# Performance work log

Hardware: AMD Instinct MI355X
Metric: run time of the kernel (lower is better)

The kernel has to match this reference:

```python
import jax, jax.numpy as jnp
import numpy as np

# --- static config (from init_kwargs) ---
B = 256        # num graphs
NPG = 128      # nodes per graph
EPG = 512      # edges per graph
DIN = 128      # dim_node
D = 256        # dim_hidden
RATIO = 0.5    # causal_ratio
N_RES = int(RATIO * EPG)
BN_EPS = 1e-5


def setup_inputs() -> dict:
    key = jax.random.key(0)
    ks = jax.random.split(key, 24)
    N = B * NPG
    x = jax.random.normal(ks[0], (N, DIN), jnp.float32)
    # edges confined within each graph, contiguous per graph (graph-sorted)
    src = jax.random.randint(ks[1], (B, EPG), 0, NPG)
    dst = jax.random.randint(ks[2], (B, EPG), 0, NPG)
    off = (jnp.arange(B, dtype=jnp.int32) * NPG)[:, None]
    edge_index = jnp.stack([(src + off).reshape(-1), (dst + off).reshape(-1)], 0).astype(jnp.int32)
    batch = jnp.repeat(jnp.arange(B, dtype=jnp.int32), NPG)

    s = 0.05
    def rn(k, shape):
        return jax.random.normal(k, shape, jnp.float32) * s
    p = dict(
        x=x, edge_index=edge_index, batch=batch,
        vemb=rn(ks[3], (1, D)),
        # conv1 GIN mlp: Linear(DIN,2D) -> BN -> ReLU -> Linear(2D,D)
        W1a=rn(ks[4], (DIN, 2 * D)), b1a=jnp.zeros((2 * D,)),
        g1a=jnp.ones((2 * D,)), be1a=jnp.zeros((2 * D,)),
        W1b=rn(ks[5], (2 * D, D)), b1b=jnp.zeros((D,)),
        g1=jnp.ones((D,)), be1=jnp.zeros((D,)),          # outer batch_norm1
        # conv2 GIN mlp
        W2a=rn(ks[6], (D, 2 * D)), b2a=jnp.zeros((2 * D,)),
        g2a=jnp.ones((2 * D,)), be2a=jnp.zeros((2 * D,)),
        W2b=rn(ks[7], (2 * D, D)), b2b=jnp.zeros((D,)),
        g2=jnp.ones((D,)), be2=jnp.zeros((D,)),          # outer batch_norm2
        # edge scorer: Linear(2D, 1)
        Wl=rn(ks[8], (2 * D, 1)), bl=jnp.zeros((1,)),
    )
    return p


def _bn(h, g, b):
    mu = h.mean(0)
    var = jnp.mean((h - mu) ** 2, 0)
    return (h - mu) * jax.lax.rsqrt(var + BN_EPS) * g + b


def reference(x, edge_index, batch, vemb,
              W1a, b1a, g1a, be1a, W1b, b1b, g1, be1,
              W2a, b2a, g2a, be2a, W2b, b2b, g2, be2,
              Wl, bl):
    N = x.shape[0]
    row, col = edge_index[0], edge_index[1]

    def gin(h, Wa, ba, ga, bta, Wb, bb):
        # GINConv, eps=0: mlp(h + sum_{j->i} h_j), aggregate src feats at dst
        agg = jax.ops.segment_sum(h[row], col, num_segments=N)
        z = (h + agg) @ Wa + ba
        z = jax.nn.relu(_bn(z, ga, bta))
        return z @ Wb + bb

    # layer 1: conv1 -> bn -> relu (dropout_rate = 0)
    post = jax.nn.relu(_bn(gin(x, W1a, b1a, g1a, be1a, W1b, b1b), g1, be1))
    # virtual node gather (embedding of index 0, one per graph)
    vfeat = jnp.broadcast_to(vemb[0], (B, D))
    post = post + vfeat[batch]
    # layer 2 (last): conv2 -> bn, no relu
    xn = _bn(gin(post, W2a, b2a, g2a, be2a, W2b, b2b), g2, be2)

    # edge scoring
    erep = jnp.concatenate([xn[row], xn[col]], axis=-1)          # [E, 2D]
    pred = (erep @ Wl + bl.astype(erep.dtype)).reshape(-1)       # [E]

    # per-graph top-k split (equal EPG edges per graph)
    pw = pred.reshape(B, EPG)
    order = jnp.argsort(-pw, axis=1)
    idx_r, idx_d = order[:, :N_RES], order[:, N_RES:]
    causal_w = jnp.take_along_axis(pw, idx_r, 1).reshape(-1)
    conf_w = -jnp.take_along_axis(pw, idx_d, 1).reshape(-1)
    ei = edge_index.reshape(2, B, EPG)
    causal_ei = jnp.take_along_axis(ei, jnp.broadcast_to(idx_r[None], (2, B, N_RES)), axis=2).reshape(2, -1)
    conf_ei = jnp.take_along_axis(ei, jnp.broadcast_to(idx_d[None], (2, B, EPG - N_RES)), axis=2).reshape(2, -1)
    return (causal_ei, causal_w, conf_ei, conf_w, pred)
```

## Files before the change

### kernel.cpp

```cpp
#include <hip/hip_runtime.h>

#define BGR   256
#define NPG   128
#define EPG   512
#define DIN   128
#define DD    256
#define DD2   512
#define NTOT  (BGR * NPG)
#define ETOT  (BGR * EPG)
#define NRES  (EPG / 2)
#define NCHUNK 256
#define MP    136

#define OFF_CEI  0
#define OFF_CW   (2 * BGR * NRES)
#define OFF_FEI  (OFF_CW + BGR * NRES)
#define OFF_FW   (OFF_FEI + 2 * BGR * NRES)
#define OFF_PRED (OFF_FW + BGR * NRES)

typedef unsigned short ushortt;
typedef __attribute__((ext_vector_type(4))) unsigned short us4;
typedef __attribute__((ext_vector_type(8))) unsigned short us8;
typedef __attribute__((ext_vector_type(8))) short short8;
typedef __attribute__((ext_vector_type(4))) float f32x4;

__device__ __forceinline__ ushortt f2bf(float f) {
    unsigned int u = __float_as_uint(f);
    unsigned int r = (u + 0x7fffu + ((u >> 16) & 1u)) >> 16;
    return (ushortt)r;
}
__device__ __forceinline__ float bf2f(ushortt u) {
    return __uint_as_float(((unsigned int)u) << 16);
}

__device__ __forceinline__ void g2lds16(const void* g, void* l) {
    __builtin_amdgcn_global_load_lds(
        (const __attribute__((address_space(1))) unsigned int*)g,
        (__attribute__((address_space(3))) unsigned int*)l, 16, 0, 0);
}

__global__ __launch_bounds__(256) void prep(const float* __restrict__ W1a,
                                            const float* __restrict__ W1b,
                                            const float* __restrict__ W2a,
                                            const float* __restrict__ W2b,
                                            const int* __restrict__ ei,
                                            ushortt* __restrict__ Wt1a,
                                            ushortt* __restrict__ Wt1b,
                                            ushortt* __restrict__ Wt2a,
                                            ushortt* __restrict__ Wt2b,
                                            ushortt* __restrict__ Madj) {
    __shared__ int cnt[NPG * NPG];
    const int t = threadIdx.x;
    if (blockIdx.x < 1792) {
        const int idx = blockIdx.x * 256 + t;
        if (idx < 65536) {
            const int k = idx >> 9, n = idx & 511;
            Wt1a[n * DIN + k] = f2bf(W1a[idx]);
        } else if (idx < 196608) {
            const int i = idx - 65536;
            const int k = i >> 8, n = i & 255;
            Wt1b[n * DD2 + k] = f2bf(W1b[i]);
        } else if (idx < 327680) {
            const int i = idx - 196608;
            const int k = i >> 9, n = i & 511;
            Wt2a[n * DD + k] = f2bf(W2a[i]);
        } else if (idx < 458752) {
            const int i = idx - 327680;
            const int k = i >> 8, n = i & 255;
            Wt2b[n * DD2 + k] = f2bf(W2b[i]);
        }
        return;
    }
    const int b = blockIdx.x - 1792;
    for (int i = t; i < NPG * NPG; i += 256) cnt[i] = 0;
    __syncthreads();
    for (int e = t; e < EPG; e += 256) {
        const int src = ei[b * EPG + e] - b * NPG;
        const int dst = ei[ETOT + b * EPG + e] - b * NPG;
        atomicAdd(&cnt[dst * NPG + src], 1);
    }
    __syncthreads();
#pragma unroll
    for (int k = 0; k < 8; ++k) {
        const int i0 = (t + k * 256) * 8;
        us8 o;
#pragma unroll
        for (int e = 0; e < 8; ++e) {
            const int i = i0 + e;
            const int v = cnt[i] + (((i >> 7) == (i & 127)) ? 1 : 0);
            o[e] = f2bf((float)v);
        }
        *(us8*)&Madj[(size_t)b * NPG * NPG + i0] = o;
    }
}

__global__ __launch_bounds__(256) void agg1_mm(const float* __restrict__ x,
                                               const ushortt* __restrict__ Madj,
                                               ushortt* __restrict__ s1) {
    __shared__ ushortt Ms[NPG * MP];
    __shared__ ushortt XT[DIN * MP];
    const int b = blockIdx.x, t = threadIdx.x;
    const int wave = t >> 6, lane = t & 63;
    const int qd = lane >> 4, r = lane & 15;
    const ushortt* Mg = Madj + (size_t)b * NPG * NPG;
#pragma unroll
    for (int k = 0; k < 8; ++k) {
        const int ch = t + k * 256;
        const int m = ch >> 4, sc = (ch & 15) * 8;
        *(us8*)&Ms[m * MP + sc] = *(const us8*)&Mg[m * NPG + sc];
    }
#pragma unroll 4
    for (int it = 0; it < 64; ++it) {
        const int s = it * 2 + (t >> 7);
        const int c = t & 127;
        XT[c * MP + s] = f2bf(x[(size_t)(b * NPG + s) * DIN + c]);
    }
    __syncthreads();
    const int wm = (wave >> 1) * 64, wn = (wave & 1) * 64;
    f32x4 acc[4][4] = {};
#pragma unroll
    for (int ks = 0; ks < 4; ++ks) {
        const int k0 = ks * 32 + qd * 8;
        short8 af[4], bfr[4];
#pragma unroll
        for (int i = 0; i < 4; ++i)
            af[i] = *(const short8*)&Ms[(wm + i * 16 + r) * MP + k0];
#pragma unroll
        for (int j = 0; j < 4; ++j)
            bfr[j] = *(const short8*)&XT[(wn + j * 16 + r) * MP + k0];
#pragma unroll
        for (int i = 0; i < 4; ++i)
#pragma unroll
            for (int j = 0; j < 4; ++j)
                acc[i][j] = __builtin_amdgcn_mfma_f32_16x16x32_bf16(af[i], bfr[j], acc[i][j], 0, 0, 0);
    }
    __syncthreads();
    ushortt* Cs = Ms;
#pragma unroll
    for (int j = 0; j < 4; ++j) {
        const int coll = wn + j * 16 + r;
#pragma unroll
        for (int i = 0; i < 4; ++i)
#pragma unroll
            for (int tt = 0; tt < 4; ++tt)
                Cs[(wm + i * 16 + qd * 4 + tt) * DIN + coll] = f2bf(acc[i][j][tt]);
    }
    __syncthreads();
#pragma unroll
    for (int k = 0; k < 8; ++k) {
        const int ch = t + k * 256;
        const int row = ch >> 4, colc = (ch & 15) * 8;
        *(us8*)&s1[(size_t)(b * NPG + row) * DIN + colc] = *(const us8*)&Cs[row * DIN + colc];
    }
}

__global__ __launch_bounds__(256) void agg2_mm(const ushortt* __restrict__ h,
                                               const float* __restrict__ psum,
                                               const float* __restrict__ psumsq,
                                               const float* __restrict__ g,
                                               const float* __restrict__ be,
                                               const float* __restrict__ vemb,
                                               const ushortt* __restrict__ Madj,
                                               ushortt* __restrict__ s2) {
    __shared__ ushortt Ms[NPG * MP];
    __shared__ ushortt PT[NPG * MP];
    __shared__ double redS[2][128];
    __shared__ double redQ[2][128];
    __shared__ float scs[128], shs[128];
    const int nb = blockIdx.x, b = blockIdx.y, t = threadIdx.x;
    const int wave = t >> 6, lane = t & 63;
    const int qd = lane >> 4, r = lane & 15;
    const ushortt* Mg = Madj + (size_t)b * NPG * NPG;
#pragma unroll
    for (int k = 0; k < 8; ++k) {
        const int ch = t + k * 256;
        const int m = ch >> 4, sc = (ch & 15) * 8;
        *(us8*)&Ms[m * MP + sc] = *(const us8*)&Mg[m * NPG + sc];
    }
    {
        const int cl = t & 127, half = t >> 7;
        const int c = nb * 128 + cl;
        double s = 0.0, q = 0.0;
#pragma unroll 4
        for (int k = half * 128; k < half * 128 + 128; ++k) {
            s += (double)psum[(size_t)k * DD + c];
            q += (double)psumsq[(size_t)k * DD + c];
        }
        redS[half][cl] = s;
        redQ[half][cl] = q;
    }
    __syncthreads();
    if (t < 128) {
        const int c = nb * 128 + t;
        const double s = redS[0][t] + redS[1][t];
        const double q = redQ[0][t] + redQ[1][t];
        const double mean = s / (double)NTOT;
        const double var = q / (double)NTOT - mean * mean;
        const double rs = 1.0 / sqrt(var + 1e-5);
        const float sc = (float)((double)g[c] * rs);
        scs[t] = sc;
        shs[t] = (float)((double)be[c] - mean * (double)sc);
    }
    __syncthreads();
    const int cl = t & 127;
    const int c = nb * 128 + cl;
    const float scv = scs[cl], shv = shs[cl], vev = vemb[c];
#pragma unroll 4
    for (int it = 0; it < 64; ++it) {
        const int s = it * 2 + (t >> 7);
        float v = fmaf(bf2f(h[(size_t)(b * NPG + s) * DD + c]), scv, shv);
        PT[cl * MP + s] = f2bf(fmaxf(v, 0.0f) + vev);
    }
    __syncthreads();
    const int wm = (wave >> 1) * 64, wn = (wave & 1) * 64;
    f32x4 acc[4][4] = {};
#pragma unroll
    for (int ks = 0; ks < 4; ++ks) {
        const int k0 = ks * 32 + qd * 8;
        short8 af[4], bfr[4];
#pragma unroll
        for (int i = 0; i < 4; ++i)
            af[i] = *(const short8*)&Ms[(wm + i * 16 + r) * MP + k0];
#pragma unroll
        for (int j = 0; j < 4; ++j)
            bfr[j] = *(const short8*)&PT[(wn + j * 16 + r) * MP + k0];
#pragma unroll
        for (int i = 0; i < 4; ++i)
#pragma unroll
            for (int j = 0; j < 4; ++j)
                acc[i][j] = __builtin_amdgcn_mfma_f32_16x16x32_bf16(af[i], bfr[j], acc[i][j], 0, 0, 0);
    }
    __syncthreads();
    ushortt* Cs = Ms;
#pragma unroll
    for (int j = 0; j < 4; ++j) {
        const int coll = wn + j * 16 + r;
#pragma unroll
        for (int i = 0; i < 4; ++i)
#pragma unroll
            for (int tt = 0; tt < 4; ++tt)
                Cs[(wm + i * 16 + qd * 4 + tt) * 128 + coll] = f2bf(acc[i][j][tt]);
    }
    __syncthreads();
#pragma unroll
    for (int k = 0; k < 8; ++k) {
        const int ch = t + k * 256;
        const int row = ch >> 4, colc = (ch & 15) * 8;
        *(us8*)&s2[(size_t)(b * NPG + row) * DD + nb * 128 + colc] =
            *(const us8*)&Cs[row * 128 + colc];
    }
}

#define BM 128
#define BN 128
#define BK 32
__global__ __launch_bounds__(256) void gemm_mfma(const ushortt* __restrict__ A,
                                                 const ushortt* __restrict__ Wt,
                                                 const float* __restrict__ bias,
                                                 ushortt* __restrict__ C,
                                                 float* __restrict__ psum,
                                                 float* __restrict__ psumsq,
                                                 int M, int N, int K) {
    __shared__ ushortt As[BM * BK];
    __shared__ ushortt Bs[BN * BK];
    __shared__ ushortt Cs[BM * BN];
    __shared__ float redS[2][BN];
    __shared__ float redQ[2][BN];
    const int tid  = threadIdx.x;
    const int wave = tid >> 6;
    const int lane = tid & 63;
    const int qd = lane >> 4;
    const int r  = lane & 15;
    const int wm = (wave >> 1) * 64;
    const int wn = (wave & 1) * 64;
    const int m0 = blockIdx.y * BM;
    const int n0 = blockIdx.x * BN;

    f32x4 acc[4][4] = {};

    for (int k0 = 0; k0 < K; k0 += BK) {
#pragma unroll
        for (int s = 0; s < 2; ++s) {
            const int o   = wave * 128 + s * 64 + lane;
            const int row = o >> 2;
            const int cg  = o & 3;
            g2lds16(A  + (size_t)(m0 + row) * K + k0 + cg * 8,
                    &As[(size_t)(wave * 128 + s * 64) * 8]);
            g2lds16(Wt + (size_t)(n0 + row) * K + k0 + cg * 8,
                    &Bs[(size_t)(wave * 128 + s * 64) * 8]);
        }
        __syncthreads();
        short8 af[4], bfr[4];
#pragma unroll
        for (int i = 0; i < 4; ++i)
            af[i] = *(const short8*)&As[(wm + i * 16 + r) * BK + qd * 8];
#pragma unroll
        for (int j = 0; j < 4; ++j)
            bfr[j] = *(const short8*)&Bs[(wn + j * 16 + r) * BK + qd * 8];
#pragma unroll
        for (int i = 0; i < 4; ++i)
#pragma unroll
            for (int j = 0; j < 4; ++j)
                acc[i][j] = __builtin_amdgcn_mfma_f32_16x16x32_bf16(af[i], bfr[j], acc[i][j], 0, 0, 0);
        __syncthreads();
    }

#pragma unroll
    for (int j = 0; j < 4; ++j) {
        const int coll = wn + j * 16 + r;
        const float bv = bias[n0 + coll];
        float s = 0.0f, q = 0.0f;
#pragma unroll
        for (int i = 0; i < 4; ++i) {
#pragma unroll
            for (int t = 0; t < 4; ++t) {
                const float v = acc[i][j][t] + bv;
                Cs[(wm + i * 16 + qd * 4 + t) * BN + coll] = f2bf(v);
                s += v;
                q = fmaf(v, v, q);
            }
        }
        s += __shfl_xor(s, 16); s += __shfl_xor(s, 32);
        q += __shfl_xor(q, 16); q += __shfl_xor(q, 32);
        if (qd == 0) {
            redS[wave >> 1][coll] = s;
            redQ[wave >> 1][coll] = q;
        }
    }
    __syncthreads();
    if (tid < BN) {
        psum[(size_t)blockIdx.y * N + n0 + tid]   = redS[0][tid] + redS[1][tid];
        psumsq[(size_t)blockIdx.y * N + n0 + tid] = redQ[0][tid] + redQ[1][tid];
    }
#pragma unroll
    for (int s8 = 0; s8 < 8; ++s8) {
        const int c    = tid + 256 * s8;
        const int row  = c >> 4;
        const int colc = (c & 15) * 8;
        const us8 v = *(const us8*)&Cs[row * BN + colc];
        *(us8*)&C[(size_t)(m0 + row) * N + n0 + colc] = v;
    }
}

__global__ __launch_bounds__(256) void gemm_mfma_bn(const ushortt* __restrict__ A,
                                                    const ushortt* __restrict__ Wt,
                                                    const float* __restrict__ scale,
                                                    const float* __restrict__ shift,
                                                    const float* __restrict__ bias,
                                                    ushortt* __restrict__ C,
                                                    float* __restrict__ psum,
                                                    float* __restrict__ psumsq,
                                                    int M, int N, int K) {
    __shared__ ushortt As[BM * BK];
    __shared__ ushortt Bs[BN * BK];
    __shared__ ushortt Cs[BM * BN];
    __shared__ float redS[2][BN];
    __shared__ float redQ[2][BN];
    __shared__ float scs[DD2], shs[DD2];
    const int tid  = threadIdx.x;
    const int wave = tid >> 6;
    const int lane = tid & 63;
    const int qd = lane >> 4;
    const int r  = lane & 15;
    const int wm = (wave >> 1) * 64;
    const int wn = (wave & 1) * 64;
    const int m0 = blockIdx.y * BM;
    const int n0 = blockIdx.x * BN;

    for (int i = tid; i < K; i += 256) {
        scs[i] = scale[i];
        shs[i] = shift[i];
    }
    __syncthreads();

    f32x4 acc[4][4] = {};

    for (int k0 = 0; k0 < K; k0 += BK) {
#pragma unroll
        for (int s = 0; s < 2; ++s) {
            const int o   = wave * 128 + s * 64 + lane;
            const int row = o >> 2;
            const int cg  = o & 3;
            g2lds16(Wt + (size_t)(n0 + row) * K + k0 + cg * 8,
                    &Bs[(size_t)(wave * 128 + s * 64) * 8]);
        }
#pragma unroll
        for (int s = 0; s < 2; ++s) {
            const int o   = wave * 128 + s * 64 + lane;
            const int row = o >> 2;
            const int cg  = o & 3;
            const us8 a8 = *(const us8*)&A[(size_t)(m0 + row) * K + k0 + cg * 8];
            const float4 s4a = *(const float4*)&scs[k0 + cg * 8];
            const float4 s4b = *(const float4*)&scs[k0 + cg * 8 + 4];
            const float4 h4a = *(const float4*)&shs[k0 + cg * 8];
            const float4 h4b = *(const float4*)&shs[k0 + cg * 8 + 4];
            us8 t8;
            t8[0] = f2bf(fmaxf(fmaf(bf2f(a8[0]), s4a.x, h4a.x), 0.0f));
            t8[1] = f2bf(fmaxf(fmaf(bf2f(a8[1]), s4a.y, h4a.y), 0.0f));
            t8[2] = f2bf(fmaxf(fmaf(bf2f(a8[2]), s4a.z, h4a.z), 0.0f));
            t8[3] = f2bf(fmaxf(fmaf(bf2f(a8[3]), s4a.w, h4a.w), 0.0f));
            t8[4] = f2bf(fmaxf(fmaf(bf2f(a8[4]), s4b.x, h4b.x), 0.0f));
            t8[5] = f2bf(fmaxf(fmaf(bf2f(a8[5]), s4b.y, h4b.y), 0.0f));
            t8[6] = f2bf(fmaxf(fmaf(bf2f(a8[6]), s4b.z, h4b.z), 0.0f));
            t8[7] = f2bf(fmaxf(fmaf(bf2f(a8[7]), s4b.w, h4b.w), 0.0f));
            *(us8*)&As[row * BK + cg * 8] = t8;
        }
        __syncthreads();
        short8 af[4], bfr[4];
#pragma unroll
        for (int i = 0; i < 4; ++i)
            af[i] = *(const short8*)&As[(wm + i * 16 + r) * BK + qd * 8];
#pragma unroll
        for (int j = 0; j < 4; ++j)
            bfr[j] = *(const short8*)&Bs[(wn + j * 16 + r) * BK + qd * 8];
#pragma unroll
        for (int i = 0; i < 4; ++i)
#pragma unroll
            for (int j = 0; j < 4; ++j)
                acc[i][j] = __builtin_amdgcn_mfma_f32_16x16x32_bf16(af[i], bfr[j], acc[i][j], 0, 0, 0);
        __syncthreads();
    }

#pragma unroll
    for (int j = 0; j < 4; ++j) {
        const int coll = wn + j * 16 + r;
        const float bv = bias[n0 + coll];
        float s = 0.0f, q = 0.0f;
#pragma unroll
        for (int i = 0; i < 4; ++i) {
#pragma unroll
            for (int t = 0; t < 4; ++t) {
                const float v = acc[i][j][t] + bv;
                Cs[(wm + i * 16 + qd * 4 + t) * BN + coll] = f2bf(v);
                s += v;
                q = fmaf(v, v, q);
            }
        }
        s += __shfl_xor(s, 16); s += __shfl_xor(s, 32);
        q += __shfl_xor(q, 16); q += __shfl_xor(q, 32);
        if (qd == 0) {
            redS[wave >> 1][coll] = s;
            redQ[wave >> 1][coll] = q;
        }
    }
    __syncthreads();
    if (tid < BN) {
        psum[(size_t)blockIdx.y * N + n0 + tid]   = redS[0][tid] + redS[1][tid];
        psumsq[(size_t)blockIdx.y * N + n0 + tid] = redQ[0][tid] + redQ[1][tid];
    }
#pragma unroll
    for (int s8 = 0; s8 < 8; ++s8) {
        const int c    = tid + 256 * s8;
        const int row  = c >> 4;
        const int colc = (c & 15) * 8;
        const us8 v = *(const us8*)&Cs[row * BN + colc];
        *(us8*)&C[(size_t)(m0 + row) * N + n0 + colc] = v;
    }
}

__global__ __launch_bounds__(256) void bn_finalize(const float* __restrict__ psum,
                                                   const float* __restrict__ psumsq,
                                                   const float* __restrict__ g,
                                                   const float* __restrict__ be,
                                                   int ncols,
                                                   float* __restrict__ scale,
                                                   float* __restrict__ shift) {
    const int c = blockIdx.x * 256 + threadIdx.x;
    double s = 0.0, s2 = 0.0;
    for (int k = 0; k < NCHUNK; ++k) {
        s += (double)psum[(size_t)k * ncols + c];
        s2 += (double)psumsq[(size_t)k * ncols + c];
    }
    const double mean = s / (double)NTOT;
    const double var = s2 / (double)NTOT - mean * mean;
    const double rs = 1.0 / sqrt(var + 1e-5);
    const float sc = (float)((double)g[c] * rs);
    scale[c] = sc;
    shift[c] = (float)((double)be[c] - mean * (double)sc);
}

__global__ __launch_bounds__(EPG) void sort_mega(const ushortt* __restrict__ h2,
                                                 const float* __restrict__ psum,
                                                 const float* __restrict__ psumsq,
                                                 const float* __restrict__ g,
                                                 const float* __restrict__ be,
                                                 const float* __restrict__ Wl,
                                                 const float* __restrict__ bl,
                                                 const int* __restrict__ ei,
                                                 float* __restrict__ out) {
    __shared__ double redS[2][DD];
    __shared__ double redQ[2][DD];
    __shared__ float scs[DD], shs[DD];
    __shared__ float pa[NPG], pb[NPG];
    __shared__ float pw[EPG];
    __shared__ int ord[EPG];
    const int b = blockIdx.x, t = threadIdx.x;
    {
        const int c = t & 255, half = t >> 8;
        double s = 0.0, q = 0.0;
#pragma unroll 4
        for (int k = half * 128; k < half * 128 + 128; ++k) {
            s += (double)psum[(size_t)k * DD + c];
            q += (double)psumsq[(size_t)k * DD + c];
        }
        redS[half][c] = s;
        redQ[half][c] = q;
    }
    __syncthreads();
    if (t < DD) {
        const double s = redS[0][t] + redS[1][t];
        const double q = redQ[0][t] + redQ[1][t];
        const double mean = s / (double)NTOT;
        const double var = q / (double)NTOT - mean * mean;
        const double rs = 1.0 / sqrt(var + 1e-5);
        const float sc = (float)((double)g[t] * rs);
        scs[t] = sc;
        shs[t] = (float)((double)be[t] - mean * (double)sc);
    }
    __syncthreads();
    {
        const int wave = t >> 6, lane = t & 63;
        const float4 w0 = *(const float4*)&Wl[lane * 4];
        const float4 w1 = *(const float4*)&Wl[DD + lane * 4];
        const float4 sc4 = *(const float4*)&scs[lane * 4];
        const float4 sh4 = *(const float4*)&shs[lane * 4];
        for (int n = wave; n < NPG; n += 8) {
            const us4 z4 = *(const us4*)&h2[(size_t)(b * NPG + n) * DD + lane * 4];
            const float x0 = fmaf(bf2f(z4.x), sc4.x, sh4.x);
            const float x1 = fmaf(bf2f(z4.y), sc4.y, sh4.y);
            const float x2 = fmaf(bf2f(z4.z), sc4.z, sh4.z);
            const float x3 = fmaf(bf2f(z4.w), sc4.w, sh4.w);
            float sa = x0 * w0.x + x1 * w0.y + x2 * w0.z + x3 * w0.w;
            float sb = x0 * w1.x + x1 * w1.y + x2 * w1.z + x3 * w1.w;
#pragma unroll
            for (int off = 32; off >= 1; off >>= 1) {
                sa += __shfl_down(sa, off);
                sb += __shfl_down(sb, off);
            }
            if (lane == 0) { pa[n] = sa; pb[n] = sb; }
        }
    }
    __syncthreads();
    const int rl = ei[b * EPG + t] - b * NPG;
    const int cl = ei[ETOT + b * EPG + t] - b * NPG;
    const float v = pa[rl] + pb[cl] + bl[0];
    pw[t] = v;
    out[OFF_PRED + b * EPG + t] = v;
    __syncthreads();
    int rank = 0;
#pragma unroll 8
    for (int k = 0; k < EPG; ++k) {
        const float u = pw[k];
        rank += (u > v) || (u == v && k < t);
    }
    ord[rank] = t;
    __syncthreads();
    const int j = ord[t];
    const float wv = pw[j];
    const float e0 = (float)ei[b * EPG + j];
    const float e1 = (float)ei[ETOT + b * EPG + j];
    if (t < NRES) {
        out[OFF_CEI + b * NRES + t] = e0;
        out[OFF_CEI + BGR * NRES + b * NRES + t] = e1;
        out[OFF_CW + b * NRES + t] = wv;
    } else {
        const int p = t - NRES;
        out[OFF_FEI + b * NRES + p] = e0;
        out[OFF_FEI + BGR * NRES + b * NRES + p] = e1;
        out[OFF_FW + b * NRES + p] = -wv;
    }
}

extern "C" void kernel_launch(void* const* d_in, const int* in_sizes, int n_in,
                              void* d_out, int out_size, void* d_ws, size_t ws_size,
                              hipStream_t stream) {
    (void)in_sizes; (void)n_in; (void)out_size; (void)ws_size;
    const float* x    = (const float*)d_in[0];
    const int*   ei   = (const int*)d_in[1];
    const float* vemb = (const float*)d_in[3];
    const float* W1a  = (const float*)d_in[4];
    const float* b1a  = (const float*)d_in[5];
    const float* g1a  = (const float*)d_in[6];
    const float* be1a = (const float*)d_in[7];
    const float* W1b  = (const float*)d_in[8];
    const float* b1b  = (const float*)d_in[9];
    const float* g1   = (const float*)d_in[10];
    const float* be1  = (const float*)d_in[11];
    const float* W2a  = (const float*)d_in[12];
    const float* b2a  = (const float*)d_in[13];
    const float* g2a  = (const float*)d_in[14];
    const float* be2a = (const float*)d_in[15];
    const float* W2b  = (const float*)d_in[16];
    const float* b2b  = (const float*)d_in[17];
    const float* g2   = (const float*)d_in[18];
    const float* be2  = (const float*)d_in[19];
    const float* Wl   = (const float*)d_in[20];
    const float* bl   = (const float*)d_in[21];
    float* out = (float*)d_out;

    char* wp = (char*)d_ws;
    auto alloc = [&](size_t bytes) -> char* {
        char* r = wp;
        wp += (bytes + 255) & ~(size_t)255;
        return r;
    };
    ushortt* zb    = (ushortt*)alloc((size_t)NTOT * 512 * 2);
    ushortt* bufC  = (ushortt*)alloc((size_t)NTOT * 256 * 2);
    ushortt* bufD  = (ushortt*)alloc((size_t)NTOT * 256 * 2);
    ushortt* bufS1 = (ushortt*)alloc((size_t)NTOT * 128 * 2);
    ushortt* Madj  = (ushortt*)alloc((size_t)BGR * NPG * NPG * 2);
    ushortt* Wt1a  = (ushortt*)alloc((size_t)DIN * DD2 * 2);
    ushortt* Wt1b  = (ushortt*)alloc((size_t)DD2 * DD * 2);
    ushortt* Wt2a  = (ushortt*)alloc((size_t)DD * DD2 * 2);
    ushortt* Wt2b  = (ushortt*)alloc((size_t)DD2 * DD * 2);
    float*   psum   = (float*)alloc((size_t)NCHUNK * 512 * 4);
    float*   psumsq = (float*)alloc((size_t)NCHUNK * 512 * 4);
    float*   scale  = (float*)alloc(512 * 4);
    float*   shift  = (float*)alloc(512 * 4);

    prep<<<2048, 256, 0, stream>>>(W1a, W1b, W2a, W2b, ei,
                                   Wt1a, Wt1b, Wt2a, Wt2b, Madj);

    agg1_mm<<<BGR, 256, 0, stream>>>(x, Madj, bufS1);

    gemm_mfma<<<dim3(DD2 / BN, NTOT / BM), 256, 0, stream>>>(bufS1, Wt1a, b1a, zb, psum, psumsq, NTOT, DD2, DIN);
    bn_finalize<<<2, 256, 0, stream>>>(psum, psumsq, g1a, be1a, DD2, scale, shift);

    gemm_mfma_bn<<<dim3(DD / BN, NTOT / BM), 256, 0, stream>>>(zb, Wt1b, scale, shift, b1b, bufC, psum, psumsq, NTOT, DD, DD2);

    agg2_mm<<<dim3(2, BGR), 256, 0, stream>>>(bufC, psum, psumsq, g1, be1, vemb, Madj, bufD);

    gemm_mfma<<<dim3(DD2 / BN, NTOT / BM), 256, 0, stream>>>(bufD, Wt2a, b2a, zb, psum, psumsq, NTOT, DD2, DD);
    bn_finalize<<<2, 256, 0, stream>>>(psum, psumsq, g2a, be2a, DD2, scale, shift);

    gemm_mfma_bn<<<dim3(DD / BN, NTOT / BM), 256, 0, stream>>>(zb, Wt2b, scale, shift, b2b, bufC, psum, psumsq, NTOT, DD, DD2);

    sort_mega<<<BGR, EPG, 0, stream>>>(bufC, psum, psumsq, g2, be2, Wl, bl, ei, out);
}
```

Measured before the change: 311.6 us.

## Fuse per-graph aggregation with first MLP GEMM and fold BN finalize into GEMMs

Merges adjacency construction, neighbor aggregation and the first linear layer (with bias and BN partial statistics) into one per-graph kernel for each GIN layer, so the aggregated features and the adjacency matrix stay in LDS instead of being written to and re-read from global memory. The separate bn_finalize launches are removed, and each consumer recomputes BN scale and shift from the per-graph partial sums. This cuts several kernel launches and the intermediate S1/S2/Madj traffic. In exchange it uses very large LDS footprints per block (about 104 KB and 138 KB), which limits occupancy to one block per CU, and the weight tiles are reloaded from global memory by every graph block.

```diff
diff --git a/kernel.cpp b/kernel.cpp
--- a/kernel.cpp
+++ b/kernel.cpp
@@ -9,8 +9,8 @@
 #define NTOT  (BGR * NPG)
 #define ETOT  (BGR * EPG)
 #define NRES  (EPG / 2)
-#define NCHUNK 256
 #define MP    136
+#define S2P   264
 
 #define OFF_CEI  0
 #define OFF_CW   (2 * BGR * NRES)
@@ -39,39 +39,52 @@
         (__attribute__((address_space(3))) unsigned int*)l, 16, 0, 0);
 }
 
-__global__ __launch_bounds__(256) void prep(const float* __restrict__ W1a,
-                                            const float* __restrict__ W1b,
-                                            const float* __restrict__ W2a,
-                                            const float* __restrict__ W2b,
-                                            const int* __restrict__ ei,
-                                            ushortt* __restrict__ Wt1a,
-                                            ushortt* __restrict__ Wt1b,
-                                            ushortt* __restrict__ Wt2a,
-                                            ushortt* __restrict__ Wt2b,
-                                            ushortt* __restrict__ Madj) {
-    __shared__ int cnt[NPG * NPG];
-    const int t = threadIdx.x;
-    if (blockIdx.x < 1792) {
-        const int idx = blockIdx.x * 256 + t;
-        if (idx < 65536) {
-            const int k = idx >> 9, n = idx & 511;
-            Wt1a[n * DIN + k] = f2bf(W1a[idx]);
-        } else if (idx < 196608) {
-            const int i = idx - 65536;
-            const int k = i >> 8, n = i & 255;
-            Wt1b[n * DD2 + k] = f2bf(W1b[i]);
-        } else if (idx < 327680) {
-            const int i = idx - 196608;
-            const int k = i >> 9, n = i & 511;
-            Wt2a[n * DD + k] = f2bf(W2a[i]);
-        } else if (idx < 458752) {
-            const int i = idx - 327680;
-            const int k = i >> 8, n = i & 255;
-            Wt2b[n * DD2 + k] = f2bf(W2b[i]);
-        }
-        return;
-    }
-    const int b = blockIdx.x - 1792;
+__global__ __launch_bounds__(256) void prep_w(const float* __restrict__ W1a,
+                                              const float* __restrict__ W1b,
+                                              const float* __restrict__ W2a,
+                                              const float* __restrict__ W2b,
+                                              ushortt* __restrict__ Wt1a,
+                                              ushortt* __restrict__ Wt1b,
+                                              ushortt* __restrict__ Wt2a,
+                                              ushortt* __restrict__ Wt2b) {
+    const int idx = blockIdx.x * 256 + threadIdx.x;
+    if (idx < 65536) {
+        const int k = idx >> 9, n = idx & 511;
+        Wt1a[n * DIN + k] = f2bf(W1a[idx]);
+    } else if (idx < 196608) {
+        const int i = idx - 65536;
+        const int k = i >> 8, n = i & 255;
+        Wt1b[n * DD2 + k] = f2bf(W1b[i]);
+    } else if (idx < 327680) {
+        const int i = idx - 196608;
+        const int k = i >> 9, n = i & 511;
+        Wt2a[n * DD + k] = f2bf(W2a[i]);
+    } else if (idx < 458752) {
+        const int i = idx - 327680;
+        const int k = i >> 8, n = i & 255;
+        Wt2b[n * DD2 + k] = f2bf(W2b[i]);
+    }
+}
+
+__global__ __launch_bounds__(256) void layer1_front(const float* __restrict__ x,
+                                                    const int* __restrict__ ei,
+                                                    const ushortt* __restrict__ Wt1a,
+                                                    const float* __restrict__ b1a,
+                                                    ushortt* __restrict__ z1,
+                                                    float* __restrict__ ps,
+                                                    float* __restrict__ pq) {
+    __shared__ __align__(16) char smem[106496];
+    ushortt* Ms = (ushortt*)smem;
+    ushortt* XT = (ushortt*)(smem + 34816);
+    ushortt* S1 = (ushortt*)(smem + 69632);
+    float* redS = (float*)(smem + 104448);
+    float* redQ = (float*)(smem + 105472);
+    int* cnt = (int*)(smem + 34816);
+    const int b = blockIdx.x, t = threadIdx.x;
+    const int wave = t >> 6, lane = t & 63;
+    const int qd = lane >> 4, r = lane & 15;
+    const int wm = (wave >> 1) * 64, wn = (wave & 1) * 64;
+
     for (int i = t; i < NPG * NPG; i += 256) cnt[i] = 0;
     __syncthreads();
     for (int e = t; e < EPG; e += 256) {
@@ -82,33 +95,16 @@
     __syncthreads();
 #pragma unroll
     for (int k = 0; k < 8; ++k) {
-        const int i0 = (t + k * 256) * 8;
-        us8 o;
-#pragma unroll
-        for (int e = 0; e < 8; ++e) {
-            const int i = i0 + e;
-            const int v = cnt[i] + (((i >> 7) == (i & 127)) ? 1 : 0);
-            o[e] = f2bf((float)v);
-        }
-        *(us8*)&Madj[(size_t)b * NPG * NPG + i0] = o;
-    }
-}
-
-__global__ __launch_bounds__(256) void agg1_mm(const float* __restrict__ x,
-                                               const ushortt* __restrict__ Madj,
-                                               ushortt* __restrict__ s1) {
-    __shared__ ushortt Ms[NPG * MP];
-    __shared__ ushortt XT[DIN * MP];
-    const int b = blockIdx.x, t = threadIdx.x;
-    const int wave = t >> 6, lane = t & 63;
-    const int qd = lane >> 4, r = lane & 15;
-    const ushortt* Mg = Madj + (size_t)b * NPG * NPG;
-#pragma unroll
-    for (int k = 0; k < 8; ++k) {
         const int ch = t + k * 256;
         const int m = ch >> 4, sc = (ch & 15) * 8;
-        *(us8*)&Ms[m * MP + sc] = *(const us8*)&Mg[m * NPG + sc];
-    }
+#pragma unroll
+        for (int e = 0; e < 8; ++e) {
+            const int s = sc + e;
+            Ms[m * MP + s] = f2bf((float)(cnt[m * NPG + s] + (m == s ? 1 : 0)));
+        }
+    }
+    __syncthreads();
+
 #pragma unroll 4
     for (int it = 0; it < 64; ++it) {
         const int s = it * 2 + (t >> 7);
@@ -116,241 +112,113 @@
         XT[c * MP + s] = f2bf(x[(size_t)(b * NPG + s) * DIN + c]);
     }
     __syncthreads();
-    const int wm = (wave >> 1) * 64, wn = (wave & 1) * 64;
-    f32x4 acc[4][4] = {};
-#pragma unroll
-    for (int ks = 0; ks < 4; ++ks) {
-        const int k0 = ks * 32 + qd * 8;
-        short8 af[4], bfr[4];
-#pragma unroll
-        for (int i = 0; i < 4; ++i)
-            af[i] = *(const short8*)&Ms[(wm + i * 16 + r) * MP + k0];
-#pragma unroll
-        for (int j = 0; j < 4; ++j)
-            bfr[j] = *(const short8*)&XT[(wn + j * 16 + r) * MP + k0];
-#pragma unroll
-        for (int i = 0; i < 4; ++i)
+
+    {
+        f32x4 acc[4][4] = {};
+#pragma unroll
+        for (int ks = 0; ks < 4; ++ks) {
+            const int k0 = ks * 32 + qd * 8;
+            short8 af[4], bfr[4];
+#pragma unroll
+            for (int i = 0; i < 4; ++i)
+                af[i] = *(const short8*)&Ms[(wm + i * 16 + r) * MP + k0];
 #pragma unroll
             for (int j = 0; j < 4; ++j)
-                acc[i][j] = __builtin_amdgcn_mfma_f32_16x16x32_bf16(af[i], bfr[j], acc[i][j], 0, 0, 0);
-    }
-    __syncthreads();
+                bfr[j] = *(const short8*)&XT[(wn + j * 16 + r) * MP + k0];
+#pragma unroll
+            for (int i = 0; i < 4; ++i)
+#pragma unroll
+                for (int j = 0; j < 4; ++j)
+                    acc[i][j] = __builtin_amdgcn_mfma_f32_16x16x32_bf16(af[i], bfr[j], acc[i][j], 0, 0, 0);
+        }
+#pragma unroll
+        for (int j = 0; j < 4; ++j) {
+            const int coll = wn + j * 16 + r;
+#pragma unroll
+            for (int i = 0; i < 4; ++i)
+#pragma unroll
+                for (int tt = 0; tt < 4; ++tt)
+                    S1[(wm + i * 16 + qd * 4 + tt) * MP + coll] = f2bf(acc[i][j][tt]);
+        }
+    }
+
+    ushortt* Wc = XT;
     ushortt* Cs = Ms;
-#pragma unroll
-    for (int j = 0; j < 4; ++j) {
-        const int coll = wn + j * 16 + r;
-#pragma unroll
-        for (int i = 0; i < 4; ++i)
-#pragma unroll
-            for (int tt = 0; tt < 4; ++tt)
-                Cs[(wm + i * 16 + qd * 4 + tt) * DIN + coll] = f2bf(acc[i][j][tt]);
-    }
-    __syncthreads();
-#pragma unroll
-    for (int k = 0; k < 8; ++k) {
-        const int ch = t + k * 256;
-        const int row = ch >> 4, colc = (ch & 15) * 8;
-        *(us8*)&s1[(size_t)(b * NPG + row) * DIN + colc] = *(const us8*)&Cs[row * DIN + colc];
-    }
-}
-
-__global__ __launch_bounds__(256) void agg2_mm(const ushortt* __restrict__ h,
-                                               const float* __restrict__ psum,
-                                               const float* __restrict__ psumsq,
-                                               const float* __restrict__ g,
-                                               const float* __restrict__ be,
-                                               const float* __restrict__ vemb,
-                                               const ushortt* __restrict__ Madj,
-                                               ushortt* __restrict__ s2) {
-    __shared__ ushortt Ms[NPG * MP];
-    __shared__ ushortt PT[NPG * MP];
-    __shared__ double redS[2][128];
-    __shared__ double redQ[2][128];
-    __shared__ float scs[128], shs[128];
-    const int nb = blockIdx.x, b = blockIdx.y, t = threadIdx.x;
-    const int wave = t >> 6, lane = t & 63;
-    const int qd = lane >> 4, r = lane & 15;
-    const ushortt* Mg = Madj + (size_t)b * NPG * NPG;
-#pragma unroll
-    for (int k = 0; k < 8; ++k) {
-        const int ch = t + k * 256;
-        const int m = ch >> 4, sc = (ch & 15) * 8;
-        *(us8*)&Ms[m * MP + sc] = *(const us8*)&Mg[m * NPG + sc];
-    }
-    {
-        const int cl = t & 127, half = t >> 7;
-        const int c = nb * 128 + cl;
-        double s = 0.0, q = 0.0;
-#pragma unroll 4
-        for (int k = half * 128; k < half * 128 + 128; ++k) {
-            s += (double)psum[(size_t)k * DD + c];
-            q += (double)psumsq[(size_t)k * DD + c];
-        }
-        redS[half][cl] = s;
-        redQ[half][cl] = q;
-    }
-    __syncthreads();
-    if (t < 128) {
-        const int c = nb * 128 + t;
-        const double s = redS[0][t] + redS[1][t];
-        const double q = redQ[0][t] + redQ[1][t];
-        const double mean = s / (double)NTOT;
-        const double var = q / (double)NTOT - mean * mean;
-        const double rs = 1.0 / sqrt(var + 1e-5);
-        const float sc = (float)((double)g[c] * rs);
-        scs[t] = sc;
-        shs[t] = (float)((double)be[c] - mean * (double)sc);
-    }
-    __syncthreads();
-    const int cl = t & 127;
-    const int c = nb * 128 + cl;
-    const float scv = scs[cl], shv = shs[cl], vev = vemb[c];
-#pragma unroll 4
-    for (int it = 0; it < 64; ++it) {
-        const int s = it * 2 + (t >> 7);
-        float v = fmaf(bf2f(h[(size_t)(b * NPG + s) * DD + c]), scv, shv);
-        PT[cl * MP + s] = f2bf(fmaxf(v, 0.0f) + vev);
-    }
-    __syncthreads();
-    const int wm = (wave >> 1) * 64, wn = (wave & 1) * 64;
-    f32x4 acc[4][4] = {};
-#pragma unroll
-    for (int ks = 0; ks < 4; ++ks) {
-        const int k0 = ks * 32 + qd * 8;
-        short8 af[4], bfr[4];
-#pragma unroll
-        for (int i = 0; i < 4; ++i)
-            af[i] = *(const short8*)&Ms[(wm + i * 16 + r) * MP + k0];
-#pragma unroll
-        for (int j = 0; j < 4; ++j)
-            bfr[j] = *(const short8*)&PT[(wn + j * 16 + r) * MP + k0];
-#pragma unroll
-        for (int i = 0; i < 4; ++i)
+    for (int nc = 0; nc < 4; ++nc) {
+        __syncthreads();
+#pragma unroll
+        for (int k = 0; k < 8; ++k) {
+            const int ch = t + k * 256;
+            const int n = ch >> 4, kc = (ch & 15) * 8;
+            *(us8*)&Wc[n * MP + kc] = *(const us8*)&Wt1a[(size_t)(nc * 128 + n) * DIN + kc];
+        }
+        __syncthreads();
+        f32x4 acc[4][4] = {};
+#pragma unroll
+        for (int ks = 0; ks < 4; ++ks) {
+            const int k0 = ks * 32 + qd * 8;
+            short8 af[4], bfr[4];
+#pragma unroll
+            for (int i = 0; i < 4; ++i)
+                af[i] = *(const short8*)&S1[(wm + i * 16 + r) * MP + k0];
 #pragma unroll
             for (int j = 0; j < 4; ++j)
-                acc[i][j] = __builtin_amdgcn_mfma_f32_16x16x32_bf16(af[i], bfr[j], acc[i][j], 0, 0, 0);
-    }
-    __syncthreads();
-    ushortt* Cs = Ms;
-#pragma unroll
-    for (int j = 0; j < 4; ++j) {
-        const int coll = wn + j * 16 + r;
-#pragma unroll
-        for (int i = 0; i < 4; ++i)
-#pragma unroll
-            for (int tt = 0; tt < 4; ++tt)
-                Cs[(wm + i * 16 + qd * 4 + tt) * 128 + coll] = f2bf(acc[i][j][tt]);
-    }
-    __syncthreads();
-#pragma unroll
-    for (int k = 0; k < 8; ++k) {
-        const int ch = t + k * 256;
-        const int row = ch >> 4, colc = (ch & 15) * 8;
-        *(us8*)&s2[(size_t)(b * NPG + row) * DD + nb * 128 + colc] =
-            *(const us8*)&Cs[row * 128 + colc];
+                bfr[j] = *(const short8*)&Wc[(wn + j * 16 + r) * MP + k0];
+#pragma unroll
+            for (int i = 0; i < 4; ++i)
+#pragma unroll
+                for (int j = 0; j < 4; ++j)
+                    acc[i][j] = __builtin_amdgcn_mfma_f32_16x16x32_bf16(af[i], bfr[j], acc[i][j], 0, 0, 0);
+        }
+#pragma unroll
+        for (int j = 0; j < 4; ++j) {
+            const int coll = wn + j * 16 + r;
+            const float bv = b1a[nc * 128 + coll];
+            float s = 0.0f, q = 0.0f;
+#pragma unroll
+            for (int i = 0; i < 4; ++i)
+#pragma unroll
+                for (int tt = 0; tt < 4; ++tt) {
+                    const float v = acc[i][j][tt] + bv;
+                    Cs[(wm + i * 16 + qd * 4 + tt) * 128 + coll] = f2bf(v);
+                    s += v;
+                    q = fmaf(v, v, q);
+                }
+            s += __shfl_xor(s, 16); s += __shfl_xor(s, 32);
+            q += __shfl_xor(q, 16); q += __shfl_xor(q, 32);
+            if (qd == 0) {
+                redS[(wave >> 1) * 128 + coll] = s;
+                redQ[(wave >> 1) * 128 + coll] = q;
+            }
+        }
+        __syncthreads();
+        if (t < 128) {
+            ps[(size_t)b * DD2 + nc * 128 + t] = redS[t] + redS[128 + t];
+            pq[(size_t)b * DD2 + nc * 128 + t] = redQ[t] + redQ[128 + t];
+        }
+#pragma unroll
+        for (int k = 0; k < 8; ++k) {
+            const int ch = t + k * 256;
+            const int row = ch >> 4, colc = (ch & 15) * 8;
+            *(us8*)&z1[(size_t)(b * NPG + row) * DD2 + nc * 128 + colc] =
+                *(const us8*)&Cs[row * 128 + colc];
+        }
     }
 }
 
 #define BM 128
 #define BN 128
 #define BK 32
-__global__ __launch_bounds__(256) void gemm_mfma(const ushortt* __restrict__ A,
-                                                 const ushortt* __restrict__ Wt,
-                                                 const float* __restrict__ bias,
-                                                 ushortt* __restrict__ C,
-                                                 float* __restrict__ psum,
-                                                 float* __restrict__ psumsq,
-                                                 int M, int N, int K) {
-    __shared__ ushortt As[BM * BK];
-    __shared__ ushortt Bs[BN * BK];
-    __shared__ ushortt Cs[BM * BN];
-    __shared__ float redS[2][BN];
-    __shared__ float redQ[2][BN];
-    const int tid  = threadIdx.x;
-    const int wave = tid >> 6;
-    const int lane = tid & 63;
-    const int qd = lane >> 4;
-    const int r  = lane & 15;
-    const int wm = (wave >> 1) * 64;
-    const int wn = (wave & 1) * 64;
-    const int m0 = blockIdx.y * BM;
-    const int n0 = blockIdx.x * BN;
-
-    f32x4 acc[4][4] = {};
-
-    for (int k0 = 0; k0 < K; k0 += BK) {
-#pragma unroll
-        for (int s = 0; s < 2; ++s) {
-            const int o   = wave * 128 + s * 64 + lane;
-            const int row = o >> 2;
-            const int cg  = o & 3;
-            g2lds16(A  + (size_t)(m0 + row) * K + k0 + cg * 8,
-                    &As[(size_t)(wave * 128 + s * 64) * 8]);
-            g2lds16(Wt + (size_t)(n0 + row) * K + k0 + cg * 8,
-                    &Bs[(size_t)(wave * 128 + s * 64) * 8]);
-        }
-        __syncthreads();
-        short8 af[4], bfr[4];
-#pragma unroll
-        for (int i = 0; i < 4; ++i)
-            af[i] = *(const short8*)&As[(wm + i * 16 + r) * BK + qd * 8];
-#pragma unroll
-        for (int j = 0; j < 4; ++j)
-            bfr[j] = *(const short8*)&Bs[(wn + j * 16 + r) * BK + qd * 8];
-#pragma unroll
-        for (int i = 0; i < 4; ++i)
-#pragma unroll
-            for (int j = 0; j < 4; ++j)
-                acc[i][j] = __builtin_amdgcn_mfma_f32_16x16x32_bf16(af[i], bfr[j], acc[i][j], 0, 0, 0);
-        __syncthreads();
-    }
-
-#pragma unroll
-    for (int j = 0; j < 4; ++j) {
-        const int coll = wn + j * 16 + r;
-        const float bv = bias[n0 + coll];
-        float s = 0.0f, q = 0.0f;
-#pragma unroll
-        for (int i = 0; i < 4; ++i) {
-#pragma unroll
-            for (int t = 0; t < 4; ++t) {
-                const float v = acc[i][j][t] + bv;
-                Cs[(wm + i * 16 + qd * 4 + t) * BN + coll] = f2bf(v);
-                s += v;
-                q = fmaf(v, v, q);
-            }
-        }
-        s += __shfl_xor(s, 16); s += __shfl_xor(s, 32);
-        q += __shfl_xor(q, 16); q += __shfl_xor(q, 32);
-        if (qd == 0) {
-            redS[wave >> 1][coll] = s;
-            redQ[wave >> 1][coll] = q;
-        }
-    }
-    __syncthreads();
-    if (tid < BN) {
-        psum[(size_t)blockIdx.y * N + n0 + tid]   = redS[0][tid] + redS[1][tid];
-        psumsq[(size_t)blockIdx.y * N + n0 + tid] = redQ[0][tid] + redQ[1][tid];
-    }
-#pragma unroll
-    for (int s8 = 0; s8 < 8; ++s8) {
-        const int c    = tid + 256 * s8;
-        const int row  = c >> 4;
-        const int colc = (c & 15) * 8;
-        const us8 v = *(const us8*)&Cs[row * BN + colc];
-        *(us8*)&C[(size_t)(m0 + row) * N + n0 + colc] = v;
-    }
-}
-
-__global__ __launch_bounds__(256) void gemm_mfma_bn(const ushortt* __restrict__ A,
-                                                    const ushortt* __restrict__ Wt,
-                                                    const float* __restrict__ scale,
-                                                    const float* __restrict__ shift,
-                                                    const float* __restrict__ bias,
-                                                    ushortt* __restrict__ C,
-                                                    float* __restrict__ psum,
-                                                    float* __restrict__ psumsq,
-                                                    int M, int N, int K) {
+__global__ __launch_bounds__(256) void gemm_bn(const ushortt* __restrict__ A,
+                                               const ushortt* __restrict__ Wt,
+                                               const float* __restrict__ psIn,
+                                               const float* __restrict__ pqIn,
+                                               const float* __restrict__ g,
+                                               const float* __restrict__ be,
+                                               const float* __restrict__ bias,
+                                               ushortt* __restrict__ C,
+                                               float* __restrict__ psOut,
+                                               float* __restrict__ pqOut) {
     __shared__ ushortt As[BM * BK];
     __shared__ ushortt Bs[BN * BK];
     __shared__ ushortt Cs[BM * BN];
@@ -366,10 +234,23 @@
     const int wn = (wave & 1) * 64;
     const int m0 = blockIdx.y * BM;
     const int n0 = blockIdx.x * BN;
-
-    for (int i = tid; i < K; i += 256) {
-        scs[i] = scale[i];
-        shs[i] = shift[i];
+    const int K = DD2, N = DD;
+
+#pragma unroll
+    for (int h = 0; h < 2; ++h) {
+        const int c = tid + h * 256;
+        double s = 0.0, q = 0.0;
+#pragma unroll 4
+        for (int k = 0; k < 256; ++k) {
+            s += (double)psIn[(size_t)k * DD2 + c];
+            q += (double)pqIn[(size_t)k * DD2 + c];
+        }
+        const double mean = s / (double)NTOT;
+        const double var = q / (double)NTOT - mean * mean;
+        const double rs = 1.0 / sqrt(var + 1e-5);
+        const float sc = (float)((double)g[c] * rs);
+        scs[c] = sc;
+        shs[c] = (float)((double)be[c] - mean * (double)sc);
     }
     __syncthreads();
 
@@ -427,7 +308,7 @@
         const float bv = bias[n0 + coll];
         float s = 0.0f, q = 0.0f;
 #pragma unroll
-        for (int i = 0; i < 4; ++i) {
+        for (int i = 0; i < 4; ++i)
 #pragma unroll
             for (int t = 0; t < 4; ++t) {
                 const float v = acc[i][j][t] + bv;
@@ -435,7 +316,6 @@
                 s += v;
                 q = fmaf(v, v, q);
             }
-        }
         s += __shfl_xor(s, 16); s += __shfl_xor(s, 32);
         q += __shfl_xor(q, 16); q += __shfl_xor(q, 32);
         if (qd == 0) {
@@ -445,8 +325,8 @@
     }
     __syncthreads();
     if (tid < BN) {
-        psum[(size_t)blockIdx.y * N + n0 + tid]   = redS[0][tid] + redS[1][tid];
-        psumsq[(size_t)blockIdx.y * N + n0 + tid] = redQ[0][tid] + redQ[1][tid];
+        psOut[(size_t)blockIdx.y * N + n0 + tid] = redS[0][tid] + redS[1][tid];
+        pqOut[(size_t)blockIdx.y * N + n0 + tid] = redQ[0][tid] + redQ[1][tid];
     }
 #pragma unroll
     for (int s8 = 0; s8 < 8; ++s8) {
@@ -458,25 +338,173 @@
     }
 }
 
-__global__ __launch_bounds__(256) void bn_finalize(const float* __restrict__ psum,
-                                                   const float* __restrict__ psumsq,
-                                                   const float* __restrict__ g,
-                                                   const float* __restrict__ be,
-                                                   int ncols,
-                                                   float* __restrict__ scale,
-                                                   float* __restrict__ shift) {
-    const int c = blockIdx.x * 256 + threadIdx.x;
-    double s = 0.0, s2 = 0.0;
-    for (int k = 0; k < NCHUNK; ++k) {
-        s += (double)psum[(size_t)k * ncols + c];
-        s2 += (double)psumsq[(size_t)k * ncols + c];
-    }
-    const double mean = s / (double)NTOT;
-    const double var = s2 / (double)NTOT - mean * mean;
-    const double rs = 1.0 / sqrt(var + 1e-5);
-    const float sc = (float)((double)g[c] * rs);
-    scale[c] = sc;
-    shift[c] = (float)((double)be[c] - mean * (double)sc);
+__global__ __launch_bounds__(256) void layer2_mid(const ushortt* __restrict__ h1,
+                                                  const int* __restrict__ ei,
+                                                  const float* __restrict__ psIn,
+                                                  const float* __restrict__ pqIn,
+                                                  const float* __restrict__ g,
+                                                  const float* __restrict__ be,
+                                                  const float* __restrict__ vemb,
+                                                  const ushortt* __restrict__ Wt2a,
+                                                  const float* __restrict__ b2a,
+                                                  ushortt* __restrict__ z2,
+                                                  float* __restrict__ ps,
+                                                  float* __restrict__ pq) {
+    __shared__ __align__(16) char smem[141312];
+    ushortt* Ms = (ushortt*)smem;
+    ushortt* PT = (ushortt*)(smem + 34816);
+    ushortt* S2 = (ushortt*)(smem + 69632);
+    float* scs  = (float*)(smem + 137216);
+    float* shs  = (float*)(smem + 138240);
+    float* redS = (float*)(smem + 139264);
+    float* redQ = (float*)(smem + 140288);
+    int* cnt = (int*)(smem + 34816);
+    const int b = blockIdx.x, t = threadIdx.x;
+    const int wave = t >> 6, lane = t & 63;
+    const int qd = lane >> 4, r = lane & 15;
+    const int wm = (wave >> 1) * 64, wn = (wave & 1) * 64;
+
+    {
+        const int c = t;
+        double s = 0.0, q = 0.0;
+#pragma unroll 4
+        for (int k = 0; k < 256; ++k) {
+            s += (double)psIn[(size_t)k * DD + c];
+            q += (double)pqIn[(size_t)k * DD + c];
+        }
+        const double mean = s / (double)NTOT;
+        const double var = q / (double)NTOT - mean * mean;
+        const double rs = 1.0 / sqrt(var + 1e-5);
+        const float sc = (float)((double)g[c] * rs);
+        scs[c] = sc;
+        shs[c] = (float)((double)be[c] - mean * (double)sc);
+    }
+    for (int i = t; i < NPG * NPG; i += 256) cnt[i] = 0;
+    __syncthreads();
+    for (int e = t; e < EPG; e += 256) {
+        const int src = ei[b * EPG + e] - b * NPG;
+        const int dst = ei[ETOT + b * EPG + e] - b * NPG;
+        atomicAdd(&cnt[dst * NPG + src], 1);
+    }
+    __syncthreads();
+#pragma unroll
+    for (int k = 0; k < 8; ++k) {
+        const int ch = t + k * 256;
+        const int m = ch >> 4, sc = (ch & 15) * 8;
+#pragma unroll
+        for (int e = 0; e < 8; ++e) {
+            const int s = sc + e;
+            Ms[m * MP + s] = f2bf((float)(cnt[m * NPG + s] + (m == s ? 1 : 0)));
+        }
+    }
+    __syncthreads();
+
+    for (int nb = 0; nb < 2; ++nb) {
+        const int cl = t & 127;
+        const int c = nb * 128 + cl;
+        const float scv = scs[c], shv = shs[c], vev = vemb[c];
+#pragma unroll 4
+        for (int it = 0; it < 64; ++it) {
+            const int s = it * 2 + (t >> 7);
+            float v = fmaf(bf2f(h1[(size_t)(b * NPG + s) * DD + c]), scv, shv);
+            PT[cl * MP + s] = f2bf(fmaxf(v, 0.0f) + vev);
+        }
+        __syncthreads();
+        f32x4 acc[4][4] = {};
+#pragma unroll
+        for (int ks = 0; ks < 4; ++ks) {
+            const int k0 = ks * 32 + qd * 8;
+            short8 af[4], bfr[4];
+#pragma unroll
+            for (int i = 0; i < 4; ++i)
+                af[i] = *(const short8*)&Ms[(wm + i * 16 + r) * MP + k0];
+#pragma unroll
+            for (int j = 0; j < 4; ++j)
+                bfr[j] = *(const short8*)&PT[(wn + j * 16 + r) * MP + k0];
+#pragma unroll
+            for (int i = 0; i < 4; ++i)
+#pragma unroll
+                for (int j = 0; j < 4; ++j)
+                    acc[i][j] = __builtin_amdgcn_mfma_f32_16x16x32_bf16(af[i], bfr[j], acc[i][j], 0, 0, 0);
+        }
+#pragma unroll
+        for (int j = 0; j < 4; ++j) {
+            const int coll = wn + j * 16 + r;
+#pragma unroll
+            for (int i = 0; i < 4; ++i)
+#pragma unroll
+                for (int tt = 0; tt < 4; ++tt)
+                    S2[(wm + i * 16 + qd * 4 + tt) * S2P + nb * 128 + coll] = f2bf(acc[i][j][tt]);
+        }
+        __syncthreads();
+    }
+
+    ushortt* Wc = PT;
+    ushortt* Cs = Ms;
+    for (int nc = 0; nc < 4; ++nc) {
+        f32x4 acc[4][4] = {};
+#pragma unroll
+        for (int kh = 0; kh < 2; ++kh) {
+            __syncthreads();
+#pragma unroll
+            for (int k = 0; k < 8; ++k) {
+                const int ch = t + k * 256;
+                const int n = ch >> 4, kc = (ch & 15) * 8;
+                *(us8*)&Wc[n * MP + kc] =
+                    *(const us8*)&Wt2a[(size_t)(nc * 128 + n) * DD + kh * 128 + kc];
+            }
+            __syncthreads();
+#pragma unroll
+            for (int ks = 0; ks < 4; ++ks) {
+                const int k0 = ks * 32 + qd * 8;
+                short8 af[4], bfr[4];
+#pragma unroll
+                for (int i = 0; i < 4; ++i)
+                    af[i] = *(const short8*)&S2[(wm + i * 16 + r) * S2P + kh * 128 + k0];
+#pragma unroll
+                for (int j = 0; j < 4; ++j)
+                    bfr[j] = *(const short8*)&Wc[(wn + j * 16 + r) * MP + k0];
+#pragma unroll
+                for (int i = 0; i < 4; ++i)
+#pragma unroll
+                    for (int j = 0; j < 4; ++j)
+                        acc[i][j] = __builtin_amdgcn_mfma_f32_16x16x32_bf16(af[i], bfr[j], acc[i][j], 0, 0, 0);
+            }
+        }
+#pragma unroll
+        for (int j = 0; j < 4; ++j) {
+            const int coll = wn + j * 16 + r;
+            const float bv = b2a[nc * 128 + coll];
+            float s = 0.0f, q = 0.0f;
+#pragma unroll
+            for (int i = 0; i < 4; ++i)
+#pragma unroll
+                for (int tt = 0; tt < 4; ++tt) {
+                    const float v = acc[i][j][tt] + bv;
+                    Cs[(wm + i * 16 + qd * 4 + tt) * 128 + coll] = f2bf(v);
+                    s += v;
+                    q = fmaf(v, v, q);
+                }
+            s += __shfl_xor(s, 16); s += __shfl_xor(s, 32);
+            q += __shfl_xor(q, 16); q += __shfl_xor(q, 32);
+            if (qd == 0) {
+                redS[(wave >> 1) * 128 + coll] = s;
+                redQ[(wave >> 1) * 128 + coll] = q;
+            }
+        }
+        __syncthreads();
+        if (t < 128) {
+            ps[(size_t)b * DD2 + nc * 128 + t] = redS[t] + redS[128 + t];
+            pq[(size_t)b * DD2 + nc * 128 + t] = redQ[t] + redQ[128 + t];
+        }
+#pragma unroll
+        for (int k = 0; k < 8; ++k) {
+            const int ch = t + k * 256;
+            const int row = ch >> 4, colc = (ch & 15) * 8;
+            *(us8*)&z2[(size_t)(b * NPG + row) * DD2 + nc * 128 + colc] =
+                *(const us8*)&Cs[row * 128 + colc];
+        }
+    }
 }
 
 __global__ __launch_bounds__(EPG) void sort_mega(const ushortt* __restrict__ h2,
@@ -606,34 +634,24 @@
     };
     ushortt* zb    = (ushortt*)alloc((size_t)NTOT * 512 * 2);
     ushortt* bufC  = (ushortt*)alloc((size_t)NTOT * 256 * 2);
-    ushortt* bufD  = (ushortt*)alloc((size_t)NTOT * 256 * 2);
-    ushortt* bufS1 = (ushortt*)alloc((size_t)NTOT * 128 * 2);
-    ushortt* Madj  = (ushortt*)alloc((size_t)BGR * NPG * NPG * 2);
     ushortt* Wt1a  = (ushortt*)alloc((size_t)DIN * DD2 * 2);
     ushortt* Wt1b  = (ushortt*)alloc((size_t)DD2 * DD * 2);
     ushortt* Wt2a  = (ushortt*)alloc((size_t)DD * DD2 * 2);
     ushortt* Wt2b  = (ushortt*)alloc((size_t)DD2 * DD * 2);
-    float*   psum   = (float*)alloc((size_t)NCHUNK * 512 * 4);
-    float*   psumsq = (float*)alloc((size_t)NCHUNK * 512 * 4);
-    float*   scale  = (float*)alloc(512 * 4);
-    float*   shift  = (float*)alloc(512 * 4);
-
-    prep<<<2048, 256, 0, stream>>>(W1a, W1b, W2a, W2b, ei,
-                                   Wt1a, Wt1b, Wt2a, Wt2b, Madj);
-
-    agg1_mm<<<BGR, 256, 0, stream>>>(x, Madj, bufS1);
-
-    gemm_mfma<<<dim3(DD2 / BN, NTOT / BM), 256, 0, stream>>>(bufS1, Wt1a, b1a, zb, psum, psumsq, NTOT, DD2, DIN);
-    bn_finalize<<<2, 256, 0, stream>>>(psum, psumsq, g1a, be1a, DD2, scale, shift);
-
-    gemm_mfma_bn<<<dim3(DD / BN, NTOT / BM), 256, 0, stream>>>(zb, Wt1b, scale, shift, b1b, bufC, psum, psumsq, NTOT, DD, DD2);
-
-    agg2_mm<<<dim3(2, BGR), 256, 0, stream>>>(bufC, psum, psumsq, g1, be1, vemb, Madj, bufD);
-
-    gemm_mfma<<<dim3(DD2 / BN, NTOT / BM), 256, 0, stream>>>(bufD, Wt2a, b2a, zb, psum, psumsq, NTOT, DD2, DD);
-    bn_finalize<<<2, 256, 0, stream>>>(psum, psumsq, g2a, be2a, DD2, scale, shift);
-
-    gemm_mfma_bn<<<dim3(DD / BN, NTOT / BM), 256, 0, stream>>>(zb, Wt2b, scale, shift, b2b, bufC, psum, psumsq, NTOT, DD, DD2);
-
-    sort_mega<<<BGR, EPG, 0, stream>>>(bufC, psum, psumsq, g2, be2, Wl, bl, ei, out);
-}
+    float*   psA   = (float*)alloc((size_t)256 * DD2 * 4);
+    float*   pqA   = (float*)alloc((size_t)256 * DD2 * 4);
+    float*   psB   = (float*)alloc((size_t)256 * DD * 4);
+    float*   pqB   = (float*)alloc((size_t)256 * DD * 4);
+
+    prep_w<<<1792, 256, 0, stream>>>(W1a, W1b, W2a, W2b, Wt1a, Wt1b, Wt2a, Wt2b);
+
+    layer1_front<<<BGR, 256, 0, stream>>>(x, ei, Wt1a, b1a, zb, psA, pqA);
+
+    gemm_bn<<<dim3(DD / BN, NTOT / BM), 256, 0, stream>>>(zb, Wt1b, psA, pqA, g1a, be1a, b1b, bufC, psB, pqB);
+
+    layer2_mid<<<BGR, 256, 0, stream>>>(bufC, ei, psB, pqB, g1, be1, vemb, Wt2a, b2a, zb, psA, pqA);
+
+    gemm_bn<<<dim3(DD / BN, NTOT / BM), 256, 0, stream>>>(zb, Wt2b, psA, pqA, g2a, be2a, b2b, bufC, psB, pqB);
+
+    sort_mega<<<BGR, EPG, 0, stream>>>(bufC, psB, pqB, g2, be2, Wl, bl, ei, out);
+}
```

Result: slower. 356.2 us (+14.3%).
